# Kernel tuning notes

Hardware: AMD Instinct MI355X
Metric: run time of the kernel (lower is better)

Reference implementation:

```python
import jax, jax.numpy as jnp
import numpy as np

B, N, F_IN, F_OUT, H = 8, 1024, 256, 256, 4
HD = F_OUT // H  # head_dim = 64
NEG_SLOPE = 0.2


def setup_inputs() -> dict:
    key = jax.random.key(0)
    k1, k2, k3 = jax.random.split(key, 3)
    x = jax.random.normal(k1, (B, N, F_IN), dtype=jnp.float32)
    adj = jnp.ones((B, N, N), dtype=jnp.int32)
    # Linear weight, stored as [in, out] so h = x @ W
    W = jax.random.normal(k2, (F_IN, F_OUT), dtype=jnp.float32) / np.sqrt(F_IN)
    # attention vector a: [H, 2*head_dim], xavier-ish init
    a = jax.random.normal(k3, (H, 2 * HD), dtype=jnp.float32) * np.sqrt(2.0 / (H + 2 * HD))
    return {"x": x, "adj": adj, "W": W, "a": a}


def reference(x, adj, W, a):
    Bq, Nq, _ = x.shape
    h = (x @ W).reshape(Bq, Nq, H, HD).transpose(0, 2, 1, 3)  # [B,H,N,HD]
    a1, a2 = a[:, :HD], a[:, HD:]  # decompose concat: e_nm = h_n.a1 + h_m.a2
    s1 = jnp.einsum('bhnd,hd->bhn', h, a1)
    s2 = jnp.einsum('bhmd,hd->bhm', h, a2)
    e = jax.nn.leaky_relu(s1[:, :, :, None] + s2[:, :, None, :], NEG_SLOPE)  # [B,H,N,N]
    e = jnp.where(adj[:, None, :, :] == 0, -jnp.inf, e)
    attention = jax.nn.softmax(e, axis=-1)
    out = jnp.einsum('bhnm,bhmd->bhnd', attention, h)
    return out.transpose(0, 2, 1, 3).reshape(Bq, Nq, H * HD)
```

## Files before the change

### kernel.cpp

```cpp
#include <hip/hip_runtime.h>
#include <math.h>

#define H 4
#define HD 64
#define NN 1024
#define BB 8
#define FIN 256
#define FOUT 256

typedef _Float16 f16x8 __attribute__((ext_vector_type(8)));
typedef _Float16 f16x4 __attribute__((ext_vector_type(4)));
typedef _Float16 f16x2 __attribute__((ext_vector_type(2)));
typedef float f32x4 __attribute__((ext_vector_type(4)));

__global__ __launch_bounds__(256) void prep(const int* __restrict__ adj,
                                            unsigned* __restrict__ adjP,
                                            const float* __restrict__ W,
                                            _Float16* __restrict__ WT) {
  __shared__ float tile[64][68];
  const int tid = threadIdx.x;
  if (blockIdx.x < 1024) {
    size_t widx = (size_t)blockIdx.x * 256 + tid;
    const int4* p = (const int4*)adj + widx * 8;
    int4 v[8];
#pragma unroll
    for (int i = 0; i < 8; ++i) v[i] = p[i];
    unsigned bits = 0;
#pragma unroll
    for (int i = 0; i < 8; ++i) {
      bits |= (v[i].x != 0 ? 1u : 0u) << (4 * i);
      bits |= (v[i].y != 0 ? 2u : 0u) << (4 * i);
      bits |= (v[i].z != 0 ? 4u : 0u) << (4 * i);
      bits |= (v[i].w != 0 ? 8u : 0u) << (4 * i);
    }
    adjP[widx] = bits;
  } else {
    const int bx = blockIdx.x - 1024;
    const int k0 = (bx & 3) * 64, f0 = (bx >> 2) * 64;
    const int r = tid >> 4, c4 = (tid & 15) * 4;
#pragma unroll
    for (int p = 0; p < 4; ++p) {
      float4 v = *(const float4*)&W[(size_t)(k0 + p * 16 + r) * FOUT + f0 + c4];
      *(float4*)&tile[p * 16 + r][c4] = v;
    }
    __syncthreads();
    const int f = tid >> 2, kg = (tid & 3) * 16;
#pragma unroll
    for (int i = 0; i < 4; ++i) {
      f16x4 o;
#pragma unroll
      for (int j = 0; j < 4; ++j) o[j] = (_Float16)tile[kg + i * 4 + j][f];
      *(f16x4*)&WT[(size_t)(f0 + f) * FIN + k0 + kg + i * 4] = o;
    }
  }
}

__global__ __launch_bounds__(256) void gemm_xw(const float* __restrict__ x,
                                               const _Float16* __restrict__ WT,
                                               const float* __restrict__ a,
                                               _Float16* __restrict__ hT,
                                               float* __restrict__ s1_ws,
                                               float* __restrict__ s2_ws) {
  __shared__ _Float16 xs[64][264];
  const int tid = threadIdx.x;
  const int lane = tid & 63, w = tid >> 6;
  const int c = lane & 15, q = lane >> 4;
  const int bn0 = blockIdx.x * 64;
  const int head = blockIdx.y;
  const int b = bn0 >> 10, nb = bn0 & 1023;
  const int bh = b * H + head;

  float4 v[16];
#pragma unroll
  for (int p = 0; p < 16; ++p) {
    int f = p * 256 + tid;
    int row = f >> 6, col = (f & 63) * 4;
    v[p] = *(const float4*)&x[(size_t)(bn0 + row) * FIN + col];
  }
#pragma unroll
  for (int p = 0; p < 16; ++p) {
    int f = p * 256 + tid;
    int row = f >> 6, col = (f & 63) * 4;
    f16x4 h4;
    h4[0] = (_Float16)v[p].x; h4[1] = (_Float16)v[p].y;
    h4[2] = (_Float16)v[p].z; h4[3] = (_Float16)v[p].w;
    *(f16x4*)&xs[row][col] = h4;
  }
  __syncthreads();

  f32x4 acc[4];
#pragma unroll
  for (int t = 0; t < 4; ++t) acc[t] = (f32x4){0.f, 0.f, 0.f, 0.f};
  const _Float16* wbase = WT + (size_t)head * 64 * FIN;
#pragma unroll
  for (int ks = 0; ks < 8; ++ks) {
    f16x8 af = *(const f16x8*)&xs[w * 16 + c][ks * 32 + q * 8];
#pragma unroll
    for (int t = 0; t < 4; ++t) {
      f16x8 bf = *(const f16x8*)&wbase[(size_t)(t * 16 + c) * FIN + ks * 32 + q * 8];
      acc[t] = __builtin_amdgcn_mfma_f32_16x16x32_f16(af, bf, acc[t], 0, 0, 0);
    }
  }

  float a1v[4], a2v[4];
#pragma unroll
  for (int t = 0; t < 4; ++t) {
    a1v[t] = a[head * 2 * HD + t * 16 + c];
    a2v[t] = a[head * 2 * HD + HD + t * 16 + c];
  }
  float s1p[4] = {0.f, 0.f, 0.f, 0.f};
  float s2p[4] = {0.f, 0.f, 0.f, 0.f};
#pragma unroll
  for (int t = 0; t < 4; ++t) {
    f16x4 hv;
#pragma unroll
    for (int rr = 0; rr < 4; ++rr) {
      hv[rr] = (_Float16)acc[t][rr];
      s1p[rr] += acc[t][rr] * a1v[t];
      s2p[rr] += acc[t][rr] * a2v[t];
    }
    *(f16x4*)&hT[((size_t)(bh * 64 + t * 16 + c)) * NN + nb + w * 16 + q * 4] = hv;
  }
#pragma unroll
  for (int rr = 0; rr < 4; ++rr) {
    float s1 = s1p[rr], s2 = s2p[rr];
#pragma unroll
    for (int off = 8; off; off >>= 1) {
      s1 += __shfl_xor(s1, off);
      s2 += __shfl_xor(s2, off);
    }
    if (c == 0) {
      int n = nb + w * 16 + q * 4 + rr;
      size_t idx = (size_t)bh * NN + n;
      s1_ws[idx] = s1;
      s2_ws[idx] = s2;
    }
  }
}

__global__ __launch_bounds__(256) void attn(const _Float16* __restrict__ hT,
                                            const float* __restrict__ s1_ws,
                                            const float* __restrict__ s2_ws,
                                            const unsigned* __restrict__ adjP,
                                            float* __restrict__ out) {
  __shared__ float s2r[NN];
  __shared__ _Float16 pt[2][16][136];
  __shared__ unsigned adjW[16][32];
  __shared__ float invL[16];
  const int tid = threadIdx.x, lane = tid & 63, w = tid >> 6;
  const int c = lane & 15, q = lane >> 4;
  const int ntile = blockIdx.x, bh = blockIdx.y;
  const int b = bh >> 2, head = bh & 3;
  const int n0 = ntile * 16;

  *(float4*)&s2r[tid * 4] = *(const float4*)&s2_ws[(size_t)bh * NN + tid * 4];
  if (tid < 128) {
    uint4 aw = *(const uint4*)&adjP[((size_t)(b * NN + n0)) * 32 + tid * 4];
    *(uint4*)&adjW[tid >> 3][(tid * 4) & 31] = aw;
  }
  __syncthreads();

  float s1v[4];
#pragma unroll
  for (int r = 0; r < 4; ++r) s1v[r] = s1_ws[(size_t)bh * NN + n0 + w * 4 + r];

  const int wc = lane >> 4;
  const int shft = (2 * lane) & 31;

  float mx[4];
#pragma unroll
  for (int r = 0; r < 4; ++r) mx[r] = -INFINITY;
#pragma unroll
  for (int ch = 0; ch < 8; ++ch) {
    float2 s2p = *(const float2*)&s2r[ch * 128 + 2 * lane];
#pragma unroll
    for (int r = 0; r < 4; ++r) {
      unsigned bits = adjW[w * 4 + r][ch * 4 + wc] >> shft;
      mx[r] = fmaxf(mx[r], (bits & 1u) ? s2p.x : -INFINITY);
      mx[r] = fmaxf(mx[r], (bits & 2u) ? s2p.y : -INFINITY);
    }
  }
  float Arow[4], Brow[4], ns1[4];
#pragma unroll
  for (int r = 0; r < 4; ++r) {
    float m = mx[r];
#pragma unroll
    for (int off = 32; off; off >>= 1) m = fmaxf(m, __shfl_xor(m, off));
    float t0 = s1v[r] + m;
    float M = fmaxf(t0, 0.2f * t0);
    Arow[r] = __expf(s1v[r] - M);
    Brow[r] = __expf(0.2f * s1v[r] - M);
    ns1[r] = -s1v[r];
  }

  float Lp[4] = {0.f, 0.f, 0.f, 0.f};
  f32x4 acc = (f32x4){0.f, 0.f, 0.f, 0.f};
  const _Float16* bptr = hT + ((size_t)bh * 64 + w * 16 + c) * NN + q * 8;

  f16x8 nbf0 = *(const f16x8*)(bptr);
  f16x8 nbf1 = *(const f16x8*)(bptr + 32);
  f16x8 nbf2 = *(const f16x8*)(bptr + 64);
  f16x8 nbf3 = *(const f16x8*)(bptr + 96);

  for (int ch = 0; ch < 8; ++ch) {
    const int buf = ch & 1;
    f16x8 bf0 = nbf0, bf1 = nbf1, bf2 = nbf2, bf3 = nbf3;
    float2 s2p = *(const float2*)&s2r[ch * 128 + 2 * lane];
    float ux = __expf(s2p.x), uy = __expf(s2p.y);
    float vx = __expf(0.2f * s2p.x), vy = __expf(0.2f * s2p.y);
#pragma unroll
    for (int r = 0; r < 4; ++r) {
      unsigned bits = adjW[w * 4 + r][ch * 4 + wc] >> shft;
      float p0 = (s2p.x >= ns1[r]) ? Arow[r] * ux : Brow[r] * vx;
      float p1 = (s2p.y >= ns1[r]) ? Arow[r] * uy : Brow[r] * vy;
      p0 = (bits & 1u) ? p0 : 0.f;
      p1 = (bits & 2u) ? p1 : 0.f;
      Lp[r] += p0 + p1;
      f16x2 pk = __builtin_bit_cast(f16x2, __builtin_amdgcn_cvt_pkrtz(p0, p1));
      *(f16x2*)&pt[buf][w * 4 + r][2 * lane] = pk;
    }
    if (ch < 7) {
      nbf0 = *(const f16x8*)(bptr + (ch + 1) * 128);
      nbf1 = *(const f16x8*)(bptr + (ch + 1) * 128 + 32);
      nbf2 = *(const f16x8*)(bptr + (ch + 1) * 128 + 64);
      nbf3 = *(const f16x8*)(bptr + (ch + 1) * 128 + 96);
    }
    __syncthreads();
    f16x8 a0 = *(const f16x8*)&pt[buf][c][q * 8];
    f16x8 a1 = *(const f16x8*)&pt[buf][c][32 + q * 8];
    f16x8 a2 = *(const f16x8*)&pt[buf][c][64 + q * 8];
    f16x8 a3 = *(const f16x8*)&pt[buf][c][96 + q * 8];
    acc = __builtin_amdgcn_mfma_f32_16x16x32_f16(a0, bf0, acc, 0, 0, 0);
    acc = __builtin_amdgcn_mfma_f32_16x16x32_f16(a1, bf1, acc, 0, 0, 0);
    acc = __builtin_amdgcn_mfma_f32_16x16x32_f16(a2, bf2, acc, 0, 0, 0);
    acc = __builtin_amdgcn_mfma_f32_16x16x32_f16(a3, bf3, acc, 0, 0, 0);
  }

  float myL = 0.f;
#pragma unroll
  for (int r = 0; r < 4; ++r) {
    float s = Lp[r];
#pragma unroll
    for (int off = 32; off; off >>= 1) s += __shfl_xor(s, off);
    if (lane == r) myL = s;
  }
  if (lane < 4) invL[w * 4 + lane] = 1.0f / myL;
  __syncthreads();
#pragma unroll
  for (int rr = 0; rr < 4; ++rr) {
    int nloc = q * 4 + rr;
    out[((size_t)(b * NN + n0 + nloc)) * FOUT + head * 64 + w * 16 + c] =
        acc[rr] * invL[nloc];
  }
}

extern "C" void kernel_launch(void* const* d_in, const int* in_sizes, int n_in,
                              void* d_out, int out_size, void* d_ws, size_t ws_size,
                              hipStream_t stream) {
  const float* x = (const float*)d_in[0];
  const int* adj = (const int*)d_in[1];
  const float* W = (const float*)d_in[2];
  const float* a = (const float*)d_in[3];
  float* out = (float*)d_out;

  char* ws = (char*)d_ws;
  _Float16* hT = (_Float16*)ws;
  _Float16* WT = (_Float16*)(ws + (size_t)4 * 1024 * 1024);
  float* s1_ws = (float*)(ws + (size_t)4 * 1024 * 1024 + 128 * 1024);
  float* s2_ws = s1_ws + (size_t)BB * H * NN;
  unsigned* adjP = (unsigned*)(s2_ws + (size_t)BB * H * NN);

  prep<<<1040, 256, 0, stream>>>(adj, adjP, W, WT);
  gemm_xw<<<dim3(128, 4), 256, 0, stream>>>(x, WT, a, hT, s1_ws, s2_ws);
  attn<<<dim3(64, 32), 256, 0, stream>>>(hT, s1_ws, s2_ws, adjP, out);
}
```

Measured before the change: 129.2 us.

## Fuse adjacency packing into GEMM launch and restructure attention with split-K MFMA

The adjacency bit-packing moves out of the prep kernel into extra blocks of the x@W GEMM launch, so the 32 MB adj read overlaps the GEMM while prep only transposes W. The attention kernel is rewritten so the probability tile is built directly in MFMA A-operand registers, with no shared-memory staging and no per-chunk barriers. Work is split across waves by d-block and K-half, with a shared-memory reduction at the end. exp(s2) and exp(0.2*s2) are precomputed once per block in LDS, at the cost of more shared memory and a final cross-wave reduction.

```diff
diff --git a/kernel.cpp b/kernel.cpp
--- a/kernel.cpp
+++ b/kernel.cpp
@@ -13,18 +13,47 @@
 typedef _Float16 f16x2 __attribute__((ext_vector_type(2)));
 typedef float f32x4 __attribute__((ext_vector_type(4)));
 
-__global__ __launch_bounds__(256) void prep(const int* __restrict__ adj,
-                                            unsigned* __restrict__ adjP,
-                                            const float* __restrict__ W,
-                                            _Float16* __restrict__ WT) {
+__global__ __launch_bounds__(256) void prep_w(const float* __restrict__ W,
+                                              _Float16* __restrict__ WT) {
   __shared__ float tile[64][68];
   const int tid = threadIdx.x;
-  if (blockIdx.x < 1024) {
-    size_t widx = (size_t)blockIdx.x * 256 + tid;
-    const int4* p = (const int4*)adj + widx * 8;
+  const int bx = blockIdx.x;
+  const int k0 = (bx & 3) * 64, f0 = (bx >> 2) * 64;
+  const int r = tid >> 4, c4 = (tid & 15) * 4;
+#pragma unroll
+  for (int p = 0; p < 4; ++p) {
+    float4 v = *(const float4*)&W[(size_t)(k0 + p * 16 + r) * FOUT + f0 + c4];
+    *(float4*)&tile[p * 16 + r][c4] = v;
+  }
+  __syncthreads();
+  const int f = tid >> 2, kg = (tid & 3) * 16;
+#pragma unroll
+  for (int i = 0; i < 4; ++i) {
+    f16x4 o;
+#pragma unroll
+    for (int j = 0; j < 4; ++j) o[j] = (_Float16)tile[kg + i * 4 + j][f];
+    *(f16x4*)&WT[(size_t)(f0 + f) * FIN + k0 + kg + i * 4] = o;
+  }
+}
+
+__global__ __launch_bounds__(256) void gemm_pack(const float* __restrict__ x,
+                                                 const _Float16* __restrict__ WT,
+                                                 const float* __restrict__ a,
+                                                 const int* __restrict__ adj,
+                                                 unsigned* __restrict__ adjP,
+                                                 _Float16* __restrict__ hT,
+                                                 float* __restrict__ s1_ws,
+                                                 float* __restrict__ s2_ws) {
+  __shared__ _Float16 xs[64][264];
+  const int tid = threadIdx.x;
+
+  if (blockIdx.x >= 128) {
+    const int p = (blockIdx.x - 128) + 256 * blockIdx.y;
+    size_t widx = (size_t)p * 256 + tid;
+    const int4* ap = (const int4*)adj + widx * 8;
     int4 v[8];
 #pragma unroll
-    for (int i = 0; i < 8; ++i) v[i] = p[i];
+    for (int i = 0; i < 8; ++i) v[i] = ap[i];
     unsigned bits = 0;
 #pragma unroll
     for (int i = 0; i < 8; ++i) {
@@ -34,35 +63,9 @@
       bits |= (v[i].w != 0 ? 8u : 0u) << (4 * i);
     }
     adjP[widx] = bits;
-  } else {
-    const int bx = blockIdx.x - 1024;
-    const int k0 = (bx & 3) * 64, f0 = (bx >> 2) * 64;
-    const int r = tid >> 4, c4 = (tid & 15) * 4;
-#pragma unroll
-    for (int p = 0; p < 4; ++p) {
-      float4 v = *(const float4*)&W[(size_t)(k0 + p * 16 + r) * FOUT + f0 + c4];
-      *(float4*)&tile[p * 16 + r][c4] = v;
-    }
-    __syncthreads();
-    const int f = tid >> 2, kg = (tid & 3) * 16;
-#pragma unroll
-    for (int i = 0; i < 4; ++i) {
-      f16x4 o;
-#pragma unroll
-      for (int j = 0; j < 4; ++j) o[j] = (_Float16)tile[kg + i * 4 + j][f];
-      *(f16x4*)&WT[(size_t)(f0 + f) * FIN + k0 + kg + i * 4] = o;
-    }
-  }
-}
-
-__global__ __launch_bounds__(256) void gemm_xw(const float* __restrict__ x,
-                                               const _Float16* __restrict__ WT,
-                                               const float* __restrict__ a,
-                                               _Float16* __restrict__ hT,
-                                               float* __restrict__ s1_ws,
-                                               float* __restrict__ s2_ws) {
-  __shared__ _Float16 xs[64][264];
-  const int tid = threadIdx.x;
+    return;
+  }
+
   const int lane = tid & 63, w = tid >> 6;
   const int c = lane & 15, q = lane >> 4;
   const int bn0 = blockIdx.x * 64;
@@ -143,114 +146,120 @@
                                             const float* __restrict__ s2_ws,
                                             const unsigned* __restrict__ adjP,
                                             float* __restrict__ out) {
-  __shared__ float s2r[NN];
-  __shared__ _Float16 pt[2][16][136];
-  __shared__ unsigned adjW[16][32];
-  __shared__ float invL[16];
+  __shared__ float s2r[NN], uu[NN], vv[NN];
+  __shared__ unsigned adjW[32][16];
+  __shared__ float maxbuf[4][16];
+  __shared__ float Lbuf[2][16];
+  __shared__ float accbuf[2][64][8];
   const int tid = threadIdx.x, lane = tid & 63, w = tid >> 6;
   const int c = lane & 15, q = lane >> 4;
   const int ntile = blockIdx.x, bh = blockIdx.y;
   const int b = bh >> 2, head = bh & 3;
   const int n0 = ntile * 16;
-
-  *(float4*)&s2r[tid * 4] = *(const float4*)&s2_ws[(size_t)bh * NN + tid * 4];
-  if (tid < 128) {
-    uint4 aw = *(const uint4*)&adjP[((size_t)(b * NN + n0)) * 32 + tid * 4];
-    *(uint4*)&adjW[tid >> 3][(tid * 4) & 31] = aw;
-  }
-  __syncthreads();
-
-  float s1v[4];
-#pragma unroll
-  for (int r = 0; r < 4; ++r) s1v[r] = s1_ws[(size_t)bh * NN + n0 + w * 4 + r];
-
-  const int wc = lane >> 4;
-  const int shft = (2 * lane) & 31;
-
-  float mx[4];
-#pragma unroll
-  for (int r = 0; r < 4; ++r) mx[r] = -INFINITY;
-#pragma unroll
-  for (int ch = 0; ch < 8; ++ch) {
-    float2 s2p = *(const float2*)&s2r[ch * 128 + 2 * lane];
-#pragma unroll
-    for (int r = 0; r < 4; ++r) {
-      unsigned bits = adjW[w * 4 + r][ch * 4 + wc] >> shft;
-      mx[r] = fmaxf(mx[r], (bits & 1u) ? s2p.x : -INFINITY);
-      mx[r] = fmaxf(mx[r], (bits & 2u) ? s2p.y : -INFINITY);
-    }
-  }
-  float Arow[4], Brow[4], ns1[4];
-#pragma unroll
-  for (int r = 0; r < 4; ++r) {
-    float m = mx[r];
-#pragma unroll
-    for (int off = 32; off; off >>= 1) m = fmaxf(m, __shfl_xor(m, off));
-    float t0 = s1v[r] + m;
-    float M = fmaxf(t0, 0.2f * t0);
-    Arow[r] = __expf(s1v[r] - M);
-    Brow[r] = __expf(0.2f * s1v[r] - M);
-    ns1[r] = -s1v[r];
-  }
-
-  float Lp[4] = {0.f, 0.f, 0.f, 0.f};
-  f32x4 acc = (f32x4){0.f, 0.f, 0.f, 0.f};
-  const _Float16* bptr = hT + ((size_t)bh * 64 + w * 16 + c) * NN + q * 8;
-
-  f16x8 nbf0 = *(const f16x8*)(bptr);
-  f16x8 nbf1 = *(const f16x8*)(bptr + 32);
-  f16x8 nbf2 = *(const f16x8*)(bptr + 64);
-  f16x8 nbf3 = *(const f16x8*)(bptr + 96);
-
-  for (int ch = 0; ch < 8; ++ch) {
-    const int buf = ch & 1;
-    f16x8 bf0 = nbf0, bf1 = nbf1, bf2 = nbf2, bf3 = nbf3;
-    float2 s2p = *(const float2*)&s2r[ch * 128 + 2 * lane];
-    float ux = __expf(s2p.x), uy = __expf(s2p.y);
-    float vx = __expf(0.2f * s2p.x), vy = __expf(0.2f * s2p.y);
-#pragma unroll
-    for (int r = 0; r < 4; ++r) {
-      unsigned bits = adjW[w * 4 + r][ch * 4 + wc] >> shft;
-      float p0 = (s2p.x >= ns1[r]) ? Arow[r] * ux : Brow[r] * vx;
-      float p1 = (s2p.y >= ns1[r]) ? Arow[r] * uy : Brow[r] * vy;
-      p0 = (bits & 1u) ? p0 : 0.f;
-      p1 = (bits & 2u) ? p1 : 0.f;
-      Lp[r] += p0 + p1;
-      f16x2 pk = __builtin_bit_cast(f16x2, __builtin_amdgcn_cvt_pkrtz(p0, p1));
-      *(f16x2*)&pt[buf][w * 4 + r][2 * lane] = pk;
-    }
-    if (ch < 7) {
-      nbf0 = *(const f16x8*)(bptr + (ch + 1) * 128);
-      nbf1 = *(const f16x8*)(bptr + (ch + 1) * 128 + 32);
-      nbf2 = *(const f16x8*)(bptr + (ch + 1) * 128 + 64);
-      nbf3 = *(const f16x8*)(bptr + (ch + 1) * 128 + 96);
-    }
-    __syncthreads();
-    f16x8 a0 = *(const f16x8*)&pt[buf][c][q * 8];
-    f16x8 a1 = *(const f16x8*)&pt[buf][c][32 + q * 8];
-    f16x8 a2 = *(const f16x8*)&pt[buf][c][64 + q * 8];
-    f16x8 a3 = *(const f16x8*)&pt[buf][c][96 + q * 8];
-    acc = __builtin_amdgcn_mfma_f32_16x16x32_f16(a0, bf0, acc, 0, 0, 0);
-    acc = __builtin_amdgcn_mfma_f32_16x16x32_f16(a1, bf1, acc, 0, 0, 0);
-    acc = __builtin_amdgcn_mfma_f32_16x16x32_f16(a2, bf2, acc, 0, 0, 0);
-    acc = __builtin_amdgcn_mfma_f32_16x16x32_f16(a3, bf3, acc, 0, 0, 0);
-  }
-
-  float myL = 0.f;
-#pragma unroll
-  for (int r = 0; r < 4; ++r) {
-    float s = Lp[r];
-#pragma unroll
-    for (int off = 32; off; off >>= 1) s += __shfl_xor(s, off);
-    if (lane == r) myL = s;
-  }
-  if (lane < 4) invL[w * 4 + lane] = 1.0f / myL;
-  __syncthreads();
-#pragma unroll
-  for (int rr = 0; rr < 4; ++rr) {
-    int nloc = q * 4 + rr;
-    out[((size_t)(b * NN + n0 + nloc)) * FOUT + head * 64 + w * 16 + c] =
-        acc[rr] * invL[nloc];
+  const int dblock = w >> 1, khalf = w & 1;
+  const int K0 = khalf * 512;
+
+  {
+    float4 s2f = *(const float4*)&s2_ws[(size_t)bh * NN + tid * 4];
+    *(float4*)&s2r[tid * 4] = s2f;
+    float4 u4 = make_float4(__expf(s2f.x), __expf(s2f.y), __expf(s2f.z), __expf(s2f.w));
+    *(float4*)&uu[tid * 4] = u4;
+    float4 v4 = make_float4(__expf(0.2f * s2f.x), __expf(0.2f * s2f.y),
+                            __expf(0.2f * s2f.z), __expf(0.2f * s2f.w));
+    *(float4*)&vv[tid * 4] = v4;
+    if (tid < 128) {
+      const int row = tid >> 3, wd0 = (tid & 7) * 4;
+      uint4 aw = *(const uint4*)&adjP[((size_t)(b * NN + n0 + row)) * 32 + wd0];
+      adjW[wd0 + 0][row] = aw.x;
+      adjW[wd0 + 1][row] = aw.y;
+      adjW[wd0 + 2][row] = aw.z;
+      adjW[wd0 + 3][row] = aw.w;
+    }
+  }
+  float s1v = s1_ws[(size_t)bh * NN + n0 + c];
+  __syncthreads();
+
+  float mx = -INFINITY;
+#pragma unroll
+  for (int kb = 0; kb < 16; ++kb) {
+    int base = K0 + kb * 32 + q * 8;
+    f32x4 sa = *(const f32x4*)&s2r[base];
+    f32x4 sb = *(const f32x4*)&s2r[base + 4];
+    unsigned bits = adjW[khalf * 16 + kb][c] >> (q * 8);
+#pragma unroll
+    for (int j = 0; j < 4; ++j) {
+      mx = fmaxf(mx, ((bits >> j) & 1u) ? sa[j] : -INFINITY);
+      mx = fmaxf(mx, ((bits >> (j + 4)) & 1u) ? sb[j] : -INFINITY);
+    }
+  }
+  mx = fmaxf(mx, __shfl_xor(mx, 16));
+  mx = fmaxf(mx, __shfl_xor(mx, 32));
+  if (lane < 16) maxbuf[w][lane] = mx;
+  __syncthreads();
+  float mrow = fmaxf(fmaxf(maxbuf[0][c], maxbuf[1][c]),
+                     fmaxf(maxbuf[2][c], maxbuf[3][c]));
+  float t0 = s1v + mrow;
+  float M = fmaxf(t0, 0.2f * t0);
+  float Arow = __expf(s1v - M);
+  float Brow = __expf(0.2f * s1v - M);
+  float ns1 = -s1v;
+
+  float Lp = 0.f;
+  f32x4 acc0 = (f32x4){0.f, 0.f, 0.f, 0.f};
+  f32x4 acc1 = (f32x4){0.f, 0.f, 0.f, 0.f};
+  const _Float16* bp0 = hT + ((size_t)bh * 64 + dblock * 32 + c) * NN + K0 + q * 8;
+  const _Float16* bp1 = bp0 + (size_t)16 * NN;
+#pragma unroll 4
+  for (int kb = 0; kb < 16; ++kb) {
+    int base = K0 + kb * 32 + q * 8;
+    f32x4 sa = *(const f32x4*)&s2r[base];
+    f32x4 sb = *(const f32x4*)&s2r[base + 4];
+    f32x4 ua = *(const f32x4*)&uu[base];
+    f32x4 ub = *(const f32x4*)&uu[base + 4];
+    f32x4 va = *(const f32x4*)&vv[base];
+    f32x4 vb = *(const f32x4*)&vv[base + 4];
+    unsigned bits = adjW[khalf * 16 + kb][c] >> (q * 8);
+    float p[8];
+#pragma unroll
+    for (int j = 0; j < 4; ++j) {
+      float pa = (sa[j] >= ns1) ? Arow * ua[j] : Brow * va[j];
+      float pb = (sb[j] >= ns1) ? Arow * ub[j] : Brow * vb[j];
+      p[j] = ((bits >> j) & 1u) ? pa : 0.f;
+      p[j + 4] = ((bits >> (j + 4)) & 1u) ? pb : 0.f;
+    }
+    Lp += ((p[0] + p[1]) + (p[2] + p[3])) + ((p[4] + p[5]) + (p[6] + p[7]));
+    union { f16x8 v8; f16x2 h2[4]; } U;
+    U.h2[0] = __builtin_bit_cast(f16x2, __builtin_amdgcn_cvt_pkrtz(p[0], p[1]));
+    U.h2[1] = __builtin_bit_cast(f16x2, __builtin_amdgcn_cvt_pkrtz(p[2], p[3]));
+    U.h2[2] = __builtin_bit_cast(f16x2, __builtin_amdgcn_cvt_pkrtz(p[4], p[5]));
+    U.h2[3] = __builtin_bit_cast(f16x2, __builtin_amdgcn_cvt_pkrtz(p[6], p[7]));
+    f16x8 bf0 = *(const f16x8*)(bp0 + kb * 32);
+    f16x8 bf1 = *(const f16x8*)(bp1 + kb * 32);
+    acc0 = __builtin_amdgcn_mfma_f32_16x16x32_f16(U.v8, bf0, acc0, 0, 0, 0);
+    acc1 = __builtin_amdgcn_mfma_f32_16x16x32_f16(U.v8, bf1, acc1, 0, 0, 0);
+  }
+
+  Lp += __shfl_xor(Lp, 16);
+  Lp += __shfl_xor(Lp, 32);
+  if (w < 2 && lane < 16) Lbuf[w][lane] = Lp;
+  if (khalf == 1) {
+    *(f32x4*)&accbuf[dblock][lane][0] = acc0;
+    *(f32x4*)&accbuf[dblock][lane][4] = acc1;
+  }
+  __syncthreads();
+  if (khalf == 0) {
+    f32x4 o0 = *(const f32x4*)&accbuf[dblock][lane][0];
+    f32x4 o1 = *(const f32x4*)&accbuf[dblock][lane][4];
+    acc0 += o0;
+    acc1 += o1;
+#pragma unroll
+    for (int rr = 0; rr < 4; ++rr) {
+      int row = q * 4 + rr;
+      float il = 1.0f / (Lbuf[0][row] + Lbuf[1][row]);
+      size_t o = ((size_t)(b * NN + n0 + row)) * FOUT + head * 64 + dblock * 32;
+      out[o + c] = acc0[rr] * il;
+      out[o + 16 + c] = acc1[rr] * il;
+    }
   }
 }
 
@@ -270,7 +279,7 @@
   float* s2_ws = s1_ws + (size_t)BB * H * NN;
   unsigned* adjP = (unsigned*)(s2_ws + (size_t)BB * H * NN);
 
-  prep<<<1040, 256, 0, stream>>>(adj, adjP, W, WT);
-  gemm_xw<<<dim3(128, 4), 256, 0, stream>>>(x, WT, a, hT, s1_ws, s2_ws);
+  prep_w<<<16, 256, 0, stream>>>(W, WT);
+  gemm_pack<<<dim3(384, 4), 256, 0, stream>>>(x, WT, a, adj, adjP, hT, s1_ws, s2_ws);
   attn<<<dim3(64, 32), 256, 0, stream>>>(hT, s1_ws, s2_ws, adjP, out);
 }
```

After: 135.2 us. 4.6% more time.
